# Kernel tuning notes

Measured on AMD Instinct MI355X. Metric: run time of the kernel, lower is better.

Reference implementation:

```python
import jax, jax.numpy as jnp
import numpy as np

B, S, I, H, O = 32, 2048, 128, 512, 128


def setup_inputs() -> dict:
    key = jax.random.key(0)
    ks = jax.random.split(key, 9)
    std = 1.0 / np.sqrt(H)
    u = lambda k, shape: jax.random.uniform(k, shape, jnp.float32, -std, std)
    return {
        "x": jax.random.normal(ks[0], (B, S, I), jnp.float32),
        # layer 0 cell: gates packed as [z; r; g]
        "wx0": u(ks[1], (3 * H, I)),
        "bx0": u(ks[2], (3 * H,)),
        "wh0": u(ks[3], (3 * H, H)),
        # layer 1 cell
        "wx1": u(ks[4], (3 * H, H)),
        "bx1": u(ks[5], (3 * H,)),
        "wh1": u(ks[6], (3 * H, H)),
        # output projection why
        "wy": u(ks[7], (O, H)),
        "by": u(ks[8], (O,)),
    }


def _gru_cell(x_t, h, wx, bx, wh):
    # x_t: (B, in), h: (B, H). One GEMM for x-gates, one for h-gates.
    gx = x_t @ wx.T + bx          # (B, 3H)
    gh = h @ wh.T                 # (B, 3H)
    xz, xr, xg = jnp.split(gx, 3, axis=-1)
    hz, hr, hg = jnp.split(gh, 3, axis=-1)
    z = jax.nn.sigmoid(xz + hz)
    r = jax.nn.sigmoid(xr + hr)
    g = jnp.tanh(xg + r * hg)
    return g + z * (h - g)


def reference(x, wx0, bx0, wh0, wx1, bx1, wh1, wy, by):
    h0 = jnp.zeros((B, H), x.dtype)
    h1 = jnp.zeros((B, H), x.dtype)

    def step(carry, x_t):
        h0, h1 = carry
        h0 = _gru_cell(x_t, h0, wx0, bx0, wh0)
        h1 = _gru_cell(h0, h1, wx1, bx1, wh1)
        y = h1 @ wy.T + by        # (B, O)
        return (h0, h1), y

    (h0, h1), ys = jax.lax.scan(step, (h0, h1), jnp.swapaxes(x, 0, 1))
    layer_output = jnp.swapaxes(ys, 0, 1)            # (B, S, O)
    hidden_state = jnp.stack([h0, h1], axis=1)       # (B, L, H)
    return layer_output, hidden_state
```

## Files before the change

### kernel.cpp

```cpp
#include <hip/hip_runtime.h>
#include <stdint.h>

#define BB 32
#define SS 2048
#define II 128
#define HH 512
#define OO 128

#define NA 32
#define NB 32
#define NY 4
#define NBLK (NA + NB + NY)
#define PHASES (SS + 2)
#define THREADS 256

#define CNT_OFF 0
#define H0_OFF  16384
#define H1_OFF  (16384 + 65536)
#define WS_BYTES (16384 + 2 * 65536)

#define REDOFF 98304
#define LDS_BYTES (98304 + 6144)

typedef __attribute__((ext_vector_type(8))) short short8;
typedef __attribute__((ext_vector_type(4))) float f32x4;

__device__ __forceinline__ short f2bf(float f) {
  unsigned int u = __float_as_uint(f);
  u += 0x7fffu + ((u >> 16) & 1u);
  return (short)(u >> 16);
}
__device__ __forceinline__ float sigm(float v) { return 1.0f / (1.0f + __expf(-v)); }
__device__ __forceinline__ float tanhc(float v) {
  v = fminf(fmaxf(v, -15.0f), 15.0f);
  float e = __expf(2.0f * v);
  return (e - 1.0f) / (e + 1.0f);
}

#define LDG16(dst_, p_) \
  asm volatile("global_load_dwordx4 %0, %1, off sc0 sc1" : "=&v"(dst_) : "v"(p_))
#define STG2(p_, v_) \
  asm volatile("global_store_short %0, %1, off sc0 sc1" :: "v"(p_), "v"(v_))
#define VDRAIN() do { \
  asm volatile("s_waitcnt vmcnt(0)" ::: "memory"); \
  __builtin_amdgcn_sched_barrier(0); \
} while (0)

__global__ __launch_bounds__(THREADS, 1)
void gru_persist(const float* __restrict__ x,
                 const float* __restrict__ wx0, const float* __restrict__ bx0,
                 const float* __restrict__ wh0,
                 const float* __restrict__ wx1, const float* __restrict__ bx1,
                 const float* __restrict__ wh1,
                 const float* __restrict__ wy,  const float* __restrict__ by,
                 float* __restrict__ out, unsigned char* __restrict__ ws)
{
  extern __shared__ char smem[];
  short8* ldsw = (short8*)smem;
  float*  red  = (float*)(smem + REDOFF);

  unsigned int*   cnt    = (unsigned int*)(ws + CNT_OFF);
  unsigned short* pubH0  = (unsigned short*)(ws + H0_OFF);
  unsigned short* pubH1  = (unsigned short*)(ws + H1_OFF);

  const int tid = threadIdx.x;
  const int l   = tid & 63;
  const int wv  = tid >> 6;
  const int lr  = l & 15;
  const int lg  = l >> 4;
  const int bid = blockIdx.x;
  const int role = (bid < NA) ? 0 : (bid < NA + NB) ? 1 : 2;

  if (role == 0) {
    const int ua = bid * 16;
    for (int f = wv; f < 60; f += 4) {
      const int nt = f / 20, kt = f % 20;
      const int row = nt * 512 + ua + lr;
      const float* src = (kt < 4) ? (wx0 + (size_t)row * II + kt * 32 + lg * 8)
                                  : (wh0 + (size_t)row * HH + (kt - 4) * 32 + lg * 8);
      short8 v;
#pragma unroll
      for (int j = 0; j < 8; ++j) v[j] = f2bf(src[j]);
      ldsw[(f << 6) + l] = v;
    }
  } else if (role == 1) {
    const int ub = (bid - NA) * 16;
    for (int f = wv; f < 96; f += 4) {
      const int nt = f >> 5, kt = f & 31;
      const int row = nt * 512 + ub + lr;
      const float* src = (kt < 16) ? (wx1 + (size_t)row * HH + kt * 32 + lg * 8)
                                   : (wh1 + (size_t)row * HH + (kt - 16) * 32 + lg * 8);
      short8 v;
#pragma unroll
      for (int j = 0; j < 8; ++j) v[j] = f2bf(src[j]);
      ldsw[(f << 6) + l] = v;
    }
  } else {
    const int oy = (bid - NA - NB) * 32;
    for (int f = wv; f < 32; f += 4) {
      const int nt = f >> 4, kt = f & 15;
      const int row = oy + nt * 16 + lr;
      const float* src = wy + (size_t)row * HH + kt * 32 + lg * 8;
      short8 v;
#pragma unroll
      for (int j = 0; j < 8; ++j) v[j] = f2bf(src[j]);
      ldsw[(f << 6) + l] = v;
    }
  }
  __syncthreads();

  const int mh = wv & 1;
  const int kh = wv >> 1;
  const int bA = mh * 16 + lr;
  const int bC = mh * 16 + lg * 4;

  int u0 = 0;
  float bz = 0.f, brr = 0.f, bg = 0.f;
  if (role == 0) u0 = bid * 16;
  else if (role == 1) u0 = (bid - NA) * 16;
  if (role <= 1 && kh == 0) {
    const float* bx = role ? bx1 : bx0;
    bz  = bx[u0 + lr];
    brr = bx[512 + u0 + lr];
    bg  = bx[1024 + u0 + lr];
  }
  int oy = 0;
  const int ynt = wv >> 1;
  float byv = 0.f;
  if (role == 2) { oy = (bid - NA - NB) * 32; byv = by[oy + ynt * 16 + lr]; }

  f32x4 hm = {0.f, 0.f, 0.f, 0.f};

  for (int p = 0; p < PHASES; ++p) {
    float4 xr[4][2];
    const bool actx = (role == 0 && kh == 0 && p < SS);
    if (actx) {
      const float* xp = x + (size_t)bA * (SS * II) + (size_t)p * II;
#pragma unroll
      for (int t = 0; t < 4; ++t) {
        xr[t][0] = *(const float4*)(xp + t * 32 + lg * 8);
        xr[t][1] = *(const float4*)(xp + t * 32 + lg * 8 + 4);
      }
    }

    if (p > 0) {
      if (tid == 0) {
        while (__hip_atomic_load(&cnt[p - 1], __ATOMIC_RELAXED, __HIP_MEMORY_SCOPE_AGENT) < NBLK)
          __builtin_amdgcn_s_sleep(1);
      }
      __syncthreads();
    }

    const bool act01 = (role == 0) ? (p < SS) : (p >= 1 && p <= SS);
    if (role <= 1 && act01) {
      const unsigned short* pubA  = pubH0 + ((size_t)((p - 1) & 1)) * (BB * HH);
      const unsigned short* pubB2 = pubH1 + ((size_t)(p & 1)) * (BB * HH);

      f32x4 aZ = {0,0,0,0}, aR = {0,0,0,0}, aG1 = {0,0,0,0}, aG2 = {0,0,0,0};
      short8 pf[16];

      if (role == 0) {
        const unsigned short* pa = pubA + (size_t)bA * HH;
        if (kh == 0) {
#pragma unroll
          for (int i = 0; i < 6; ++i) LDG16(pf[i], pa + i * 32 + lg * 8);
          VDRAIN();
#pragma unroll
          for (int kt = 0; kt < 4; ++kt) {
            short8 af;
#pragma unroll
            for (int j = 0; j < 4; ++j) { af[j] = f2bf(xr[kt][0][j]); af[4 + j] = f2bf(xr[kt][1][j]); }
            short8 wz = ldsw[((0 * 20 + kt) << 6) + l];
            short8 wr = ldsw[((1 * 20 + kt) << 6) + l];
            short8 wg = ldsw[((2 * 20 + kt) << 6) + l];
            aZ  = __builtin_amdgcn_mfma_f32_16x16x32_bf16(af, wz, aZ, 0, 0, 0);
            aR  = __builtin_amdgcn_mfma_f32_16x16x32_bf16(af, wr, aR, 0, 0, 0);
            aG1 = __builtin_amdgcn_mfma_f32_16x16x32_bf16(af, wg, aG1, 0, 0, 0);
          }
#pragma unroll
          for (int kt = 4; kt < 10; ++kt) {
            short8 af = pf[kt - 4];
            short8 wz = ldsw[((0 * 20 + kt) << 6) + l];
            short8 wr = ldsw[((1 * 20 + kt) << 6) + l];
            short8 wg = ldsw[((2 * 20 + kt) << 6) + l];
            aZ  = __builtin_amdgcn_mfma_f32_16x16x32_bf16(af, wz, aZ, 0, 0, 0);
            aR  = __builtin_amdgcn_mfma_f32_16x16x32_bf16(af, wr, aR, 0, 0, 0);
            aG2 = __builtin_amdgcn_mfma_f32_16x16x32_bf16(af, wg, aG2, 0, 0, 0);
          }
        } else {
#pragma unroll
          for (int i = 0; i < 10; ++i) LDG16(pf[i], pa + (6 + i) * 32 + lg * 8);
          VDRAIN();
#pragma unroll
          for (int kt = 10; kt < 20; ++kt) {
            short8 af = pf[kt - 10];
            short8 wz = ldsw[((0 * 20 + kt) << 6) + l];
            short8 wr = ldsw[((1 * 20 + kt) << 6) + l];
            short8 wg = ldsw[((2 * 20 + kt) << 6) + l];
            aZ  = __builtin_amdgcn_mfma_f32_16x16x32_bf16(af, wz, aZ, 0, 0, 0);
            aR  = __builtin_amdgcn_mfma_f32_16x16x32_bf16(af, wr, aR, 0, 0, 0);
            aG2 = __builtin_amdgcn_mfma_f32_16x16x32_bf16(af, wg, aG2, 0, 0, 0);
          }
        }
      } else {
        if (kh == 0) {
          const unsigned short* pa = pubA + (size_t)bA * HH;
#pragma unroll
          for (int i = 0; i < 16; ++i) LDG16(pf[i], pa + i * 32 + lg * 8);
          VDRAIN();
#pragma unroll
          for (int kt = 0; kt < 16; ++kt) {
            short8 af = pf[kt];
            short8 wz = ldsw[((0 * 32 + kt) << 6) + l];
            short8 wr = ldsw[((1 * 32 + kt) << 6) + l];
            short8 wg = ldsw[((2 * 32 + kt) << 6) + l];
            aZ  = __builtin_amdgcn_mfma_f32_16x16x32_bf16(af, wz, aZ, 0, 0, 0);
            aR  = __builtin_amdgcn_mfma_f32_16x16x32_bf16(af, wr, aR, 0, 0, 0);
            aG1 = __builtin_amdgcn_mfma_f32_16x16x32_bf16(af, wg, aG1, 0, 0, 0);
          }
        } else {
          const unsigned short* pb = pubB2 + (size_t)bA * HH;
#pragma unroll
          for (int i = 0; i < 16; ++i) LDG16(pf[i], pb + i * 32 + lg * 8);
          VDRAIN();
#pragma unroll
          for (int kt = 16; kt < 32; ++kt) {
            short8 af = pf[kt - 16];
            short8 wz = ldsw[((0 * 32 + kt) << 6) + l];
            short8 wr = ldsw[((1 * 32 + kt) << 6) + l];
            short8 wg = ldsw[((2 * 32 + kt) << 6) + l];
            aZ  = __builtin_amdgcn_mfma_f32_16x16x32_bf16(af, wz, aZ, 0, 0, 0);
            aR  = __builtin_amdgcn_mfma_f32_16x16x32_bf16(af, wr, aR, 0, 0, 0);
            aG2 = __builtin_amdgcn_mfma_f32_16x16x32_bf16(af, wg, aG2, 0, 0, 0);
          }
        }
      }

      if (kh == 1) {
#pragma unroll
        for (int r = 0; r < 4; ++r) {
          red[((mh * 3 + 0) * 4 + r) * 64 + l] = aZ[r];
          red[((mh * 3 + 1) * 4 + r) * 64 + l] = aR[r];
          red[((mh * 3 + 2) * 4 + r) * 64 + l] = aG2[r];
        }
      }
      __syncthreads();
      if (kh == 0) {
        unsigned short* pubO = role ? (pubH1 + ((size_t)((p - 1) & 1)) * (BB * HH))
                                    : (pubH0 + ((size_t)(p & 1)) * (BB * HH));
        const bool fin = role ? (p == SS) : (p == SS - 1);
#pragma unroll
        for (int r = 0; r < 4; ++r) {
          const float z2 = red[((mh * 3 + 0) * 4 + r) * 64 + l];
          const float r2 = red[((mh * 3 + 1) * 4 + r) * 64 + l];
          const float g2 = red[((mh * 3 + 2) * 4 + r) * 64 + l];
          const float zz = sigm(aZ[r] + z2 + bz);
          const float rr = sigm(aR[r] + r2 + brr);
          const float gg = tanhc(aG1[r] + bg + rr * (aG2[r] + g2));
          const float hn = gg + zz * (hm[r] - gg);
          hm[r] = hn;
          unsigned short* pp = pubO + (size_t)(bC + r) * HH + u0 + lr;
          int hv = (int)(unsigned short)f2bf(hn);
          STG2(pp, hv);
          if (fin)
            out[(size_t)(BB * SS * OO) + (size_t)(bC + r) * (2 * HH) + (role ? HH : 0) + u0 + lr] = hn;
        }
      }
    } else if (role == 2 && p >= 2) {
      const unsigned short* pubV = pubH1 + ((size_t)(p & 1)) * (BB * HH) + (size_t)bA * HH;
      f32x4 acc = {0,0,0,0};
      short8 pf[16];
#pragma unroll
      for (int i = 0; i < 16; ++i) LDG16(pf[i], pubV + i * 32 + lg * 8);
      VDRAIN();
#pragma unroll
      for (int kt = 0; kt < 16; ++kt) {
        short8 bw = ldsw[((ynt * 16 + kt) << 6) + l];
        acc = __builtin_amdgcn_mfma_f32_16x16x32_bf16(pf[kt], bw, acc, 0, 0, 0);
      }
#pragma unroll
      for (int r = 0; r < 4; ++r) {
        out[(size_t)(bC + r) * (SS * OO) + (size_t)(p - 2) * OO + oy + ynt * 16 + lr] = acc[r] + byv;
      }
    }

    VDRAIN();
    __syncthreads();
    if (tid == 0)
      __hip_atomic_fetch_add(&cnt[p], 1u, __ATOMIC_RELAXED, __HIP_MEMORY_SCOPE_AGENT);
  }
}

extern "C" void kernel_launch(void* const* d_in, const int* in_sizes, int n_in,
                              void* d_out, int out_size, void* d_ws, size_t ws_size,
                              hipStream_t stream) {
  (void)in_sizes; (void)n_in; (void)out_size;
  const float* x   = (const float*)d_in[0];
  const float* wx0 = (const float*)d_in[1];
  const float* bx0 = (const float*)d_in[2];
  const float* wh0 = (const float*)d_in[3];
  const float* wx1 = (const float*)d_in[4];
  const float* bx1 = (const float*)d_in[5];
  const float* wh1 = (const float*)d_in[6];
  const float* wy  = (const float*)d_in[7];
  const float* by  = (const float*)d_in[8];
  float* out = (float*)d_out;

  hipMemsetAsync(d_ws, 0, WS_BYTES, stream);
  gru_persist<<<dim3(NBLK), dim3(THREADS), LDS_BYTES, stream>>>(
      x, wx0, bx0, wh0, wx1, bx1, wh1, wy, by, out, (unsigned char*)d_ws);
  (void)ws_size;
}
```

Before: 13.84 ms.

## Replace global barrier with tagged hidden-state polling and per-wave flags

```diff
diff --git a/kernel.cpp b/kernel.cpp
--- a/kernel.cpp
+++ b/kernel.cpp
@@ -7,23 +7,25 @@
 #define HH 512
 #define OO 128
 
-#define NA 32
-#define NB 32
-#define NY 4
-#define NBLK (NA + NB + NY)
+#define N0 16
+#define N1 32
+#define NYB 4
+#define NBLK (N0 + N1 + NYB)
 #define PHASES (SS + 2)
 #define THREADS 256
 
-#define CNT_OFF 0
-#define H0_OFF  16384
-#define H1_OFF  (16384 + 65536)
-#define WS_BYTES (16384 + 2 * 65536)
-
-#define REDOFF 98304
-#define LDS_BYTES (98304 + 6144)
+#define FLAGS_OFF 0
+#define H0_OFF    4096
+#define H1_OFF    (4096 + 262144)
+#define WS_BYTES  (4096 + 2 * 262144)
+#define SLOT_W    (BB * HH)
+
+#define REDOFF    (120 * 1024)
+#define LDS_BYTES (120 * 1024 + 6144)
 
 typedef __attribute__((ext_vector_type(8))) short short8;
 typedef __attribute__((ext_vector_type(4))) float f32x4;
+typedef __attribute__((ext_vector_type(4))) unsigned int u32x4;
 
 __device__ __forceinline__ short f2bf(float f) {
   unsigned int u = __float_as_uint(f);
@@ -37,14 +39,52 @@
   return (e - 1.0f) / (e + 1.0f);
 }
 
-#define LDG16(dst_, p_) \
-  asm volatile("global_load_dwordx4 %0, %1, off sc0 sc1" : "=&v"(dst_) : "v"(p_))
-#define STG2(p_, v_) \
-  asm volatile("global_store_short %0, %1, off sc0 sc1" :: "v"(p_), "v"(v_))
+#define LDG4T(dst_, p_) asm volatile("global_load_dwordx4 %0, %1, off sc0 sc1" : "=&v"(dst_) : "v"(p_))
+#define STG4(p_, v_)    asm volatile("global_store_dword %0, %1, off sc0 sc1" :: "v"(p_), "v"(v_))
 #define VDRAIN() do { \
   asm volatile("s_waitcnt vmcnt(0)" ::: "memory"); \
   __builtin_amdgcn_sched_barrier(0); \
 } while (0)
+
+__device__ __forceinline__ short8 mk_af(u32x4 a, u32x4 b) {
+  short8 r;
+#pragma unroll
+  for (int j = 0; j < 4; ++j) { r[j] = (short)(a[j] >> 16); r[4 + j] = (short)(b[j] >> 16); }
+  return r;
+}
+__device__ __forceinline__ short8 mk_af_x(float4 a, float4 b) {
+  short8 r;
+  r[0] = f2bf(a.x); r[1] = f2bf(a.y); r[2] = f2bf(a.z); r[3] = f2bf(a.w);
+  r[4] = f2bf(b.x); r[5] = f2bf(b.y); r[6] = f2bf(b.z); r[7] = f2bf(b.w);
+  return r;
+}
+
+__device__ __forceinline__ void poll16(const unsigned int* p0, unsigned int tag, u32x4* pw) {
+  for (;;) {
+#pragma unroll
+    for (int i = 0; i < 16; ++i) {
+      LDG4T(pw[2 * i],     p0 + i * 32);
+      LDG4T(pw[2 * i + 1], p0 + i * 32 + 4);
+    }
+    VDRAIN();
+    unsigned int a = 0xFFFFFFFFu;
+#pragma unroll
+    for (int i = 0; i < 32; ++i) a &= pw[i][0] & pw[i][1] & pw[i][2] & pw[i][3];
+    if (__all((int)((a & 0xFFFFu) == tag))) return;
+  }
+}
+
+__device__ __forceinline__ void guard_wait(const unsigned int* flags, int l, unsigned int thresh, u32x4 gf) {
+  for (;;) {
+    unsigned int m0 = gf[0] < gf[1] ? gf[0] : gf[1];
+    unsigned int m1 = gf[2] < gf[3] ? gf[2] : gf[3];
+    unsigned int mn = m0 < m1 ? m0 : m1;
+    bool ok = (l >= NBLK) || (mn >= thresh);
+    if (__all((int)ok)) return;
+    LDG4T(gf, flags + l * 4);
+    VDRAIN();
+  }
+}
 
 __global__ __launch_bounds__(THREADS, 1)
 void gru_persist(const float* __restrict__ x,
@@ -59,9 +99,9 @@
   short8* ldsw = (short8*)smem;
   float*  red  = (float*)(smem + REDOFF);
 
-  unsigned int*   cnt    = (unsigned int*)(ws + CNT_OFF);
-  unsigned short* pubH0  = (unsigned short*)(ws + H0_OFF);
-  unsigned short* pubH1  = (unsigned short*)(ws + H1_OFF);
+  unsigned int* flags = (unsigned int*)(ws + FLAGS_OFF);
+  unsigned int* pub0  = (unsigned int*)(ws + H0_OFF);
+  unsigned int* pub1  = (unsigned int*)(ws + H1_OFF);
 
   const int tid = threadIdx.x;
   const int l   = tid & 63;
@@ -69,13 +109,16 @@
   const int lr  = l & 15;
   const int lg  = l >> 4;
   const int bid = blockIdx.x;
-  const int role = (bid < NA) ? 0 : (bid < NA + NB) ? 1 : 2;
+  const int role = (bid < N0) ? 0 : (bid < N0 + N1) ? 1 : 2;
+  const int mh = wv & 1;
+  const int bA = mh * 16 + lr;
+  const int bC = mh * 16 + lg * 4;
+  unsigned int* myflag = flags + bid * 4 + wv;
 
   if (role == 0) {
-    const int ua = bid * 16;
-    for (int f = wv; f < 60; f += 4) {
-      const int nt = f / 20, kt = f % 20;
-      const int row = nt * 512 + ua + lr;
+    for (int f = wv; f < 120; f += 4) {
+      const int uh = f / 60, g = (f % 60) / 20, kt = f % 20;
+      const int row = g * 512 + bid * 32 + uh * 16 + lr;
       const float* src = (kt < 4) ? (wx0 + (size_t)row * II + kt * 32 + lg * 8)
                                   : (wh0 + (size_t)row * HH + (kt - 4) * 32 + lg * 8);
       short8 v;
@@ -84,10 +127,10 @@
       ldsw[(f << 6) + l] = v;
     }
   } else if (role == 1) {
-    const int ub = (bid - NA) * 16;
+    const int ub = (bid - N0) * 16;
     for (int f = wv; f < 96; f += 4) {
-      const int nt = f >> 5, kt = f & 31;
-      const int row = nt * 512 + ub + lr;
+      const int g = f >> 5, kt = f & 31;
+      const int row = g * 512 + ub + lr;
       const float* src = (kt < 16) ? (wx1 + (size_t)row * HH + kt * 32 + lg * 8)
                                    : (wh1 + (size_t)row * HH + (kt - 16) * 32 + lg * 8);
       short8 v;
@@ -96,7 +139,7 @@
       ldsw[(f << 6) + l] = v;
     }
   } else {
-    const int oy = (bid - NA - NB) * 32;
+    const int oy = (bid - N0 - N1) * 32;
     for (int f = wv; f < 32; f += 4) {
       const int nt = f >> 4, kt = f & 15;
       const int row = oy + nt * 16 + lr;
@@ -109,134 +152,103 @@
   }
   __syncthreads();
 
-  const int mh = wv & 1;
-  const int kh = wv >> 1;
-  const int bA = mh * 16 + lr;
-  const int bC = mh * 16 + lg * 4;
-
-  int u0 = 0;
-  float bz = 0.f, brr = 0.f, bg = 0.f;
-  if (role == 0) u0 = bid * 16;
-  else if (role == 1) u0 = (bid - NA) * 16;
-  if (role <= 1 && kh == 0) {
-    const float* bx = role ? bx1 : bx0;
-    bz  = bx[u0 + lr];
-    brr = bx[512 + u0 + lr];
-    bg  = bx[1024 + u0 + lr];
-  }
-  int oy = 0;
-  const int ynt = wv >> 1;
-  float byv = 0.f;
-  if (role == 2) { oy = (bid - NA - NB) * 32; byv = by[oy + ynt * 16 + lr]; }
-
-  f32x4 hm = {0.f, 0.f, 0.f, 0.f};
-
-  for (int p = 0; p < PHASES; ++p) {
-    float4 xr[4][2];
-    const bool actx = (role == 0 && kh == 0 && p < SS);
-    if (actx) {
-      const float* xp = x + (size_t)bA * (SS * II) + (size_t)p * II;
+  if (role == 0) {
+    const int uh  = wv >> 1;
+    const int u0w = bid * 32 + uh * 16;
+    const int fb  = uh * 60;
+    const float bz = bx0[u0w + lr], br = bx0[512 + u0w + lr], bg = bx0[1024 + u0w + lr];
+    f32x4 hm = {0.f, 0.f, 0.f, 0.f};
+    for (int p = 0; p < PHASES; ++p) {
+      if (p >= SS) { STG4(myflag, (unsigned)(p + 1)); continue; }
+      const float* xp = x + (size_t)bA * (SS * II) + (size_t)p * II + lg * 8;
+      float4 xa[4], xb[4];
 #pragma unroll
       for (int t = 0; t < 4; ++t) {
-        xr[t][0] = *(const float4*)(xp + t * 32 + lg * 8);
-        xr[t][1] = *(const float4*)(xp + t * 32 + lg * 8 + 4);
-      }
-    }
-
-    if (p > 0) {
-      if (tid == 0) {
-        while (__hip_atomic_load(&cnt[p - 1], __ATOMIC_RELAXED, __HIP_MEMORY_SCOPE_AGENT) < NBLK)
-          __builtin_amdgcn_s_sleep(1);
-      }
-      __syncthreads();
-    }
-
-    const bool act01 = (role == 0) ? (p < SS) : (p >= 1 && p <= SS);
-    if (role <= 1 && act01) {
-      const unsigned short* pubA  = pubH0 + ((size_t)((p - 1) & 1)) * (BB * HH);
-      const unsigned short* pubB2 = pubH1 + ((size_t)(p & 1)) * (BB * HH);
-
+        xa[t] = *(const float4*)(xp + t * 32);
+        xb[t] = *(const float4*)(xp + t * 32 + 4);
+      }
+      u32x4 gf = {0, 0, 0, 0};
+      if (p >= 3) LDG4T(gf, flags + l * 4);
+      u32x4 pw[32];
+      poll16(pub0 + ((p - 1) & 3) * SLOT_W + bA * HH + lg * 8, (unsigned)p, pw);
+      STG4(myflag, (unsigned)(p + 1));
       f32x4 aZ = {0,0,0,0}, aR = {0,0,0,0}, aG1 = {0,0,0,0}, aG2 = {0,0,0,0};
-      short8 pf[16];
-
-      if (role == 0) {
-        const unsigned short* pa = pubA + (size_t)bA * HH;
-        if (kh == 0) {
-#pragma unroll
-          for (int i = 0; i < 6; ++i) LDG16(pf[i], pa + i * 32 + lg * 8);
-          VDRAIN();
-#pragma unroll
-          for (int kt = 0; kt < 4; ++kt) {
-            short8 af;
-#pragma unroll
-            for (int j = 0; j < 4; ++j) { af[j] = f2bf(xr[kt][0][j]); af[4 + j] = f2bf(xr[kt][1][j]); }
-            short8 wz = ldsw[((0 * 20 + kt) << 6) + l];
-            short8 wr = ldsw[((1 * 20 + kt) << 6) + l];
-            short8 wg = ldsw[((2 * 20 + kt) << 6) + l];
-            aZ  = __builtin_amdgcn_mfma_f32_16x16x32_bf16(af, wz, aZ, 0, 0, 0);
-            aR  = __builtin_amdgcn_mfma_f32_16x16x32_bf16(af, wr, aR, 0, 0, 0);
-            aG1 = __builtin_amdgcn_mfma_f32_16x16x32_bf16(af, wg, aG1, 0, 0, 0);
-          }
-#pragma unroll
-          for (int kt = 4; kt < 10; ++kt) {
-            short8 af = pf[kt - 4];
-            short8 wz = ldsw[((0 * 20 + kt) << 6) + l];
-            short8 wr = ldsw[((1 * 20 + kt) << 6) + l];
-            short8 wg = ldsw[((2 * 20 + kt) << 6) + l];
-            aZ  = __builtin_amdgcn_mfma_f32_16x16x32_bf16(af, wz, aZ, 0, 0, 0);
-            aR  = __builtin_amdgcn_mfma_f32_16x16x32_bf16(af, wr, aR, 0, 0, 0);
-            aG2 = __builtin_amdgcn_mfma_f32_16x16x32_bf16(af, wg, aG2, 0, 0, 0);
-          }
-        } else {
-#pragma unroll
-          for (int i = 0; i < 10; ++i) LDG16(pf[i], pa + (6 + i) * 32 + lg * 8);
-          VDRAIN();
-#pragma unroll
-          for (int kt = 10; kt < 20; ++kt) {
-            short8 af = pf[kt - 10];
-            short8 wz = ldsw[((0 * 20 + kt) << 6) + l];
-            short8 wr = ldsw[((1 * 20 + kt) << 6) + l];
-            short8 wg = ldsw[((2 * 20 + kt) << 6) + l];
-            aZ  = __builtin_amdgcn_mfma_f32_16x16x32_bf16(af, wz, aZ, 0, 0, 0);
-            aR  = __builtin_amdgcn_mfma_f32_16x16x32_bf16(af, wr, aR, 0, 0, 0);
-            aG2 = __builtin_amdgcn_mfma_f32_16x16x32_bf16(af, wg, aG2, 0, 0, 0);
-          }
+#pragma unroll
+      for (int kt = 0; kt < 4; ++kt) {
+        short8 af = mk_af_x(xa[kt], xb[kt]);
+        short8 wz = ldsw[((fb + kt) << 6) + l];
+        short8 wr = ldsw[((fb + 20 + kt) << 6) + l];
+        short8 wg = ldsw[((fb + 40 + kt) << 6) + l];
+        aZ  = __builtin_amdgcn_mfma_f32_16x16x32_bf16(af, wz, aZ, 0, 0, 0);
+        aR  = __builtin_amdgcn_mfma_f32_16x16x32_bf16(af, wr, aR, 0, 0, 0);
+        aG1 = __builtin_amdgcn_mfma_f32_16x16x32_bf16(af, wg, aG1, 0, 0, 0);
+      }
+#pragma unroll
+      for (int i = 0; i < 16; ++i) {
+        const int kt = 4 + i;
+        short8 af = mk_af(pw[2 * i], pw[2 * i + 1]);
+        short8 wz = ldsw[((fb + kt) << 6) + l];
+        short8 wr = ldsw[((fb + 20 + kt) << 6) + l];
+        short8 wg = ldsw[((fb + 40 + kt) << 6) + l];
+        aZ  = __builtin_amdgcn_mfma_f32_16x16x32_bf16(af, wz, aZ, 0, 0, 0);
+        aR  = __builtin_amdgcn_mfma_f32_16x16x32_bf16(af, wr, aR, 0, 0, 0);
+        aG2 = __builtin_amdgcn_mfma_f32_16x16x32_bf16(af, wg, aG2, 0, 0, 0);
+      }
+      if (p >= 3) guard_wait(flags, l, (unsigned)(p - 2), gf);
+      unsigned int* po = pub0 + (p & 3) * SLOT_W + u0w + lr;
+      const unsigned int tagO = (unsigned)(p + 1);
+#pragma unroll
+      for (int r = 0; r < 4; ++r) {
+        const float zz = sigm(aZ[r] + bz);
+        const float rr = sigm(aR[r] + br);
+        const float gg = tanhc(aG1[r] + bg + rr * aG2[r]);
+        const float hn = gg + zz * (hm[r] - gg);
+        hm[r] = hn;
+        const unsigned int w = ((unsigned int)(unsigned short)f2bf(hn) << 16) | tagO;
+        STG4(po + (size_t)(bC + r) * HH, w);
+        if (p == SS - 1)
+          out[(size_t)(BB * SS * OO) + (size_t)(bC + r) * (2 * HH) + u0w + lr] = hn;
+      }
+    }
+  } else if (role == 1) {
+    const int kh = wv >> 1;
+    const int u0 = (bid - N0) * 16;
+    float bz = 0.f, br = 0.f, bg = 0.f;
+    if (kh == 0) { bz = bx1[u0 + lr]; br = bx1[512 + u0 + lr]; bg = bx1[1024 + u0 + lr]; }
+    f32x4 hm = {0.f, 0.f, 0.f, 0.f};
+    for (int p = 0; p < PHASES; ++p) {
+      if (p < 1 || p > SS) { STG4(myflag, (unsigned)(p + 1)); continue; }
+      u32x4 gf = {0, 0, 0, 0};
+      if (kh == 0 && p >= 3) LDG4T(gf, flags + l * 4);
+      u32x4 pw[32];
+      f32x4 aZ = {0,0,0,0}, aR = {0,0,0,0}, aG1 = {0,0,0,0}, aG2 = {0,0,0,0};
+      if (kh == 0) {
+        poll16(pub0 + ((p - 1) & 3) * SLOT_W + bA * HH + lg * 8, (unsigned)p, pw);
+        STG4(myflag, (unsigned)(p + 1));
+#pragma unroll
+        for (int kt = 0; kt < 16; ++kt) {
+          short8 af = mk_af(pw[2 * kt], pw[2 * kt + 1]);
+          short8 wz = ldsw[((0 * 32 + kt) << 6) + l];
+          short8 wr = ldsw[((1 * 32 + kt) << 6) + l];
+          short8 wg = ldsw[((2 * 32 + kt) << 6) + l];
+          aZ  = __builtin_amdgcn_mfma_f32_16x16x32_bf16(af, wz, aZ, 0, 0, 0);
+          aR  = __builtin_amdgcn_mfma_f32_16x16x32_bf16(af, wr, aR, 0, 0, 0);
+          aG1 = __builtin_amdgcn_mfma_f32_16x16x32_bf16(af, wg, aG1, 0, 0, 0);
         }
       } else {
-        if (kh == 0) {
-          const unsigned short* pa = pubA + (size_t)bA * HH;
-#pragma unroll
-          for (int i = 0; i < 16; ++i) LDG16(pf[i], pa + i * 32 + lg * 8);
-          VDRAIN();
-#pragma unroll
-          for (int kt = 0; kt < 16; ++kt) {
-            short8 af = pf[kt];
-            short8 wz = ldsw[((0 * 32 + kt) << 6) + l];
-            short8 wr = ldsw[((1 * 32 + kt) << 6) + l];
-            short8 wg = ldsw[((2 * 32 + kt) << 6) + l];
-            aZ  = __builtin_amdgcn_mfma_f32_16x16x32_bf16(af, wz, aZ, 0, 0, 0);
-            aR  = __builtin_amdgcn_mfma_f32_16x16x32_bf16(af, wr, aR, 0, 0, 0);
-            aG1 = __builtin_amdgcn_mfma_f32_16x16x32_bf16(af, wg, aG1, 0, 0, 0);
-          }
-        } else {
-          const unsigned short* pb = pubB2 + (size_t)bA * HH;
-#pragma unroll
-          for (int i = 0; i < 16; ++i) LDG16(pf[i], pb + i * 32 + lg * 8);
-          VDRAIN();
-#pragma unroll
-          for (int kt = 16; kt < 32; ++kt) {
-            short8 af = pf[kt - 16];
-            short8 wz = ldsw[((0 * 32 + kt) << 6) + l];
-            short8 wr = ldsw[((1 * 32 + kt) << 6) + l];
-            short8 wg = ldsw[((2 * 32 + kt) << 6) + l];
-            aZ  = __builtin_amdgcn_mfma_f32_16x16x32_bf16(af, wz, aZ, 0, 0, 0);
-            aR  = __builtin_amdgcn_mfma_f32_16x16x32_bf16(af, wr, aR, 0, 0, 0);
-            aG2 = __builtin_amdgcn_mfma_f32_16x16x32_bf16(af, wg, aG2, 0, 0, 0);
-          }
+        poll16(pub1 + ((p - 2) & 3) * SLOT_W + bA * HH + lg * 8, (unsigned)(p - 1), pw);
+        STG4(myflag, (unsigned)(p + 1));
+#pragma unroll
+        for (int i = 0; i < 16; ++i) {
+          const int kt = 16 + i;
+          short8 af = mk_af(pw[2 * i], pw[2 * i + 1]);
+          short8 wz = ldsw[((0 * 32 + kt) << 6) + l];
+          short8 wr = ldsw[((1 * 32 + kt) << 6) + l];
+          short8 wg = ldsw[((2 * 32 + kt) << 6) + l];
+          aZ  = __builtin_amdgcn_mfma_f32_16x16x32_bf16(af, wz, aZ, 0, 0, 0);
+          aR  = __builtin_amdgcn_mfma_f32_16x16x32_bf16(af, wr, aR, 0, 0, 0);
+          aG2 = __builtin_amdgcn_mfma_f32_16x16x32_bf16(af, wg, aG2, 0, 0, 0);
         }
-      }
-
-      if (kh == 1) {
 #pragma unroll
         for (int r = 0; r < 4; ++r) {
           red[((mh * 3 + 0) * 4 + r) * 64 + l] = aZ[r];
@@ -246,55 +258,52 @@
       }
       __syncthreads();
       if (kh == 0) {
-        unsigned short* pubO = role ? (pubH1 + ((size_t)((p - 1) & 1)) * (BB * HH))
-                                    : (pubH0 + ((size_t)(p & 1)) * (BB * HH));
-        const bool fin = role ? (p == SS) : (p == SS - 1);
+        if (p >= 3) guard_wait(flags, l, (unsigned)(p - 2), gf);
+        unsigned int* po = pub1 + ((p - 1) & 3) * SLOT_W + u0 + lr;
+        const unsigned int tagO = (unsigned)p;
 #pragma unroll
         for (int r = 0; r < 4; ++r) {
           const float z2 = red[((mh * 3 + 0) * 4 + r) * 64 + l];
           const float r2 = red[((mh * 3 + 1) * 4 + r) * 64 + l];
           const float g2 = red[((mh * 3 + 2) * 4 + r) * 64 + l];
           const float zz = sigm(aZ[r] + z2 + bz);
-          const float rr = sigm(aR[r] + r2 + brr);
-          const float gg = tanhc(aG1[r] + bg + rr * (aG2[r] + g2));
+          const float rr = sigm(aR[r] + r2 + br);
+          const float gg = tanhc(aG1[r] + bg + rr * g2);
           const float hn = gg + zz * (hm[r] - gg);
           hm[r] = hn;
-          unsigned short* pp = pubO + (size_t)(bC + r) * HH + u0 + lr;
-          int hv = (int)(unsigned short)f2bf(hn);
-          STG2(pp, hv);
-          if (fin)
-            out[(size_t)(BB * SS * OO) + (size_t)(bC + r) * (2 * HH) + (role ? HH : 0) + u0 + lr] = hn;
+          const unsigned int w = ((unsigned int)(unsigned short)f2bf(hn) << 16) | tagO;
+          STG4(po + (size_t)(bC + r) * HH, w);
+          if (p == SS)
+            out[(size_t)(BB * SS * OO) + (size_t)(bC + r) * (2 * HH) + HH + u0 + lr] = hn;
         }
       }
-    } else if (role == 2 && p >= 2) {
-      const unsigned short* pubV = pubH1 + ((size_t)(p & 1)) * (BB * HH) + (size_t)bA * HH;
-      f32x4 acc = {0,0,0,0};
-      short8 pf[16];
-#pragma unroll
-      for (int i = 0; i < 16; ++i) LDG16(pf[i], pubV + i * 32 + lg * 8);
-      VDRAIN();
+    }
+  } else {
+    const int ynt = wv >> 1;
+    const int oy  = (bid - N0 - N1) * 32;
+    const float byv = by[oy + ynt * 16 + lr];
+    for (int p = 0; p < PHASES; ++p) {
+      if (p < 2) { STG4(myflag, (unsigned)(p + 1)); continue; }
+      u32x4 pw[32];
+      poll16(pub1 + ((p - 2) & 3) * SLOT_W + bA * HH + lg * 8, (unsigned)(p - 1), pw);
+      STG4(myflag, (unsigned)(p + 1));
+      f32x4 acc = {0, 0, 0, 0};
 #pragma unroll
       for (int kt = 0; kt < 16; ++kt) {
         short8 bw = ldsw[((ynt * 16 + kt) << 6) + l];
-        acc = __builtin_amdgcn_mfma_f32_16x16x32_bf16(pf[kt], bw, acc, 0, 0, 0);
-      }
-#pragma unroll
-      for (int r = 0; r < 4; ++r) {
+        acc = __builtin_amdgcn_mfma_f32_16x16x32_bf16(mk_af(pw[2 * kt], pw[2 * kt + 1]), bw, acc, 0, 0, 0);
+      }
+#pragma unroll
+      for (int r = 0; r < 4; ++r)
         out[(size_t)(bC + r) * (SS * OO) + (size_t)(p - 2) * OO + oy + ynt * 16 + lr] = acc[r] + byv;
-      }
-    }
-
-    VDRAIN();
-    __syncthreads();
-    if (tid == 0)
-      __hip_atomic_fetch_add(&cnt[p], 1u, __ATOMIC_RELAXED, __HIP_MEMORY_SCOPE_AGENT);
+    }
   }
 }
 
 extern "C" void kernel_launch(void* const* d_in, const int* in_sizes, int n_in,
                               void* d_out, int out_size, void* d_ws, size_t ws_size,
                               hipStream_t stream) {
-  (void)in_sizes; (void)n_in; (void)out_size;
+  (void)in_sizes; (void)n_in; (void)out_size; (void)ws_size;
   const float* x   = (const float*)d_in[0];
   const float* wx0 = (const float*)d_in[1];
   const float* bx0 = (const float*)d_in[2];
@@ -309,5 +318,4 @@
   hipMemsetAsync(d_ws, 0, WS_BYTES, stream);
   gru_persist<<<dim3(NBLK), dim3(THREADS), LDS_BYTES, stream>>>(
       x, wx0, bx0, wh0, wx1, bx1, wh1, wy, by, out, (unsigned char*)d_ws);
-  (void)ws_size;
-}
+}
```

Result: slower. 21.06 ms (+52.1%).
